# Optimization experiments

Hardware: AMD Instinct MI355X
Metric: run time of the kernel (lower is better)

The kernel has to match this reference:

```python
import jax, jax.numpy as jnp
import numpy as np

B, NQ, NC, C, NH, NP, DFF, HH, WW = 4, 300, 16, 256, 8, 4, 2048, 128, 128


def _ln(x, g, b):
    m = jnp.mean(x, -1, keepdims=True)
    v = jnp.mean((x - m) ** 2, -1, keepdims=True)
    return (x - m) / jnp.sqrt(v + 1e-5) * g + b


def _mha(x, wi, bi, wo, bo, n_heads):
    Bx, L, Cx = x.shape
    d = Cx // n_heads
    q, k, v = jnp.split(x @ wi.T + bi, 3, axis=-1)
    sh = lambda t: t.reshape(Bx, L, n_heads, d).transpose(0, 2, 1, 3)
    scale = float(1.0 / np.sqrt(d))
    a = jax.nn.softmax(jnp.einsum('bhqd,bhkd->bhqk', sh(q), sh(k)) * scale, axis=-1)
    o = jnp.einsum('bhqk,bhkd->bhqd', a, sh(v)).transpose(0, 2, 1, 3).reshape(Bx, L, Cx)
    return o @ wo.T + bo


def _grid_sample(im, grid):
    # im: [N, Ch, H, W]; grid: [N, L, P, 2] in [-1,1]; bilinear, zeros padding, align_corners=False
    N, Ch, H, W = im.shape
    gx = (grid[..., 0] + 1.0) * (W * 0.5) - 0.5
    gy = (grid[..., 1] + 1.0) * (H * 0.5) - 0.5
    x0 = jnp.floor(gx)
    y0 = jnp.floor(gy)
    wx1 = gx - x0
    wy1 = gy - y0
    imf = im.reshape(N, Ch, H * W)

    def gather(xi, yi):
        valid = ((xi >= 0) & (xi < W) & (yi >= 0) & (yi < H)).astype(im.dtype)
        idx = jnp.clip(yi, 0, H - 1).astype(jnp.int32) * W + jnp.clip(xi, 0, W - 1).astype(jnp.int32)
        vals = jnp.take_along_axis(imf, idx.reshape(N, 1, -1), axis=2).reshape(N, Ch, *xi.shape[1:])
        return vals * valid[:, None]

    return (gather(x0, y0) * ((1 - wx1) * (1 - wy1))[:, None]
            + gather(x0 + 1, y0) * (wx1 * (1 - wy1))[:, None]
            + gather(x0, y0 + 1) * ((1 - wx1) * wy1)[:, None]
            + gather(x0 + 1, y0 + 1) * (wx1 * wy1)[:, None])


def setup_inputs() -> dict:
    key = jax.random.key(0)
    ks = jax.random.split(key, 30)
    s = 0.02
    p = lambda k, shp: jax.random.normal(k, shp, jnp.float32) * s
    cxcy = jax.random.uniform(ks[0], (B, NQ * NC, 2), jnp.float32)
    wh = jax.random.uniform(ks[1], (B, NQ * NC, 2), jnp.float32) * 0.2 + 0.02
    return {
        'inst_query': jax.random.normal(ks[2], (B, NQ, C), jnp.float32),
        'sub_contour_query': jax.random.normal(ks[3], (B, NQ, NC, C), jnp.float32),
        'memory_feats': jax.random.normal(ks[4], (B, HH * WW, C), jnp.float32),
        'reference_boxes': jnp.concatenate([cxcy, wh], axis=-1),
        'inst_in_w': p(ks[5], (3 * C, C)), 'inst_in_b': p(ks[6], (3 * C,)),
        'inst_out_w': p(ks[7], (C, C)), 'inst_out_b': p(ks[8], (C,)),
        'sc_in_w': p(ks[9], (3 * C, C)), 'sc_in_b': p(ks[10], (3 * C,)),
        'sc_out_w': p(ks[11], (C, C)), 'sc_out_b': p(ks[12], (C,)),
        'off_w': p(ks[13], (NH * NP * 2, C)), 'off_b': p(ks[14], (NH * NP * 2,)),
        'aw_w': p(ks[15], (NH * NP, C)), 'aw_b': p(ks[16], (NH * NP,)),
        'outp_w': p(ks[17], (C, C)), 'outp_b': p(ks[18], (C,)),
        'lin1_w': p(ks[19], (DFF, C)), 'lin1_b': p(ks[20], (DFF,)),
        'lin2_w': p(ks[21], (C, DFF)), 'lin2_b': p(ks[22], (C,)),
        'n1_g': jnp.ones((C,), jnp.float32), 'n1_b': jnp.zeros((C,), jnp.float32),
        'n2_g': jnp.ones((C,), jnp.float32), 'n2_b': jnp.zeros((C,), jnp.float32),
        'n3_g': jnp.ones((C,), jnp.float32), 'n3_b': jnp.zeros((C,), jnp.float32),
        'H': HH, 'W': WW,
    }


def reference(inst_query, sub_contour_query, memory_feats, reference_boxes,
              inst_in_w, inst_in_b, inst_out_w, inst_out_b,
              sc_in_w, sc_in_b, sc_out_w, sc_out_b,
              off_w, off_b, aw_w, aw_b, outp_w, outp_b,
              lin1_w, lin1_b, lin2_w, lin2_b,
              n1_g, n1_b, n2_g, n2_b, n3_g, n3_b, H, W):
    Bx, Nq, Nc, Cx = sub_contour_query.shape
    Lq = Nq * Nc
    hd = Cx // NH
    # --- decoupled self-attention (eval mode: dropout = identity) ---
    inst_o = _mha(inst_query, inst_in_w, inst_in_b, inst_out_w, inst_out_b, NH)
    sc = sub_contour_query.transpose(0, 2, 1, 3).reshape(Bx * Nc, Nq, Cx)
    sc_o = _mha(sc, sc_in_w, sc_in_b, sc_out_w, sc_out_b, NH)
    sc_o = sc_o.reshape(Bx, Nc, Nq, Cx).transpose(0, 2, 1, 3)
    q_sa = sc_o + inst_o[:, :, None, :]
    tgt = (sub_contour_query + q_sa).reshape(Bx, Lq, Cx)
    tgt = _ln(tgt + q_sa.reshape(Bx, Lq, Cx), n1_g, n1_b)
    # --- deformable cross-attention ---
    offsets = (tgt @ off_w.T + off_b).reshape(Bx, Lq, NH, NP, 2)
    aw = jax.nn.softmax((tgt @ aw_w.T + aw_b).reshape(Bx, Lq, NH, NP), axis=-1)
    ref = reference_boxes[:, :, None, None, :]
    loc = ref[..., :2] + offsets * ref[..., 2:] * 0.5
    grid = (loc * 2.0 - 1.0).transpose(0, 2, 1, 3, 4).reshape(Bx * NH, Lq, NP, 2)
    mem = memory_feats.reshape(Bx, H, W, Cx).transpose(0, 3, 1, 2).reshape(Bx * NH, hd, H, W)
    samp = _grid_sample(mem, grid).reshape(Bx, NH, hd, Lq, NP).transpose(0, 3, 1, 4, 2)  # [B,Lq,nH,nP,hd]
    tgt2 = (samp * aw[..., None]).sum(3).reshape(Bx, Lq, Cx) @ outp_w.T + outp_b
    tgt = _ln(tgt + tgt2, n2_g, n2_b)
    # --- FFN ---
    tgt2 = jax.nn.relu(tgt @ lin1_w.T + lin1_b) @ lin2_w.T + lin2_b
    tgt = _ln(tgt + tgt2, n3_g, n3_b)
    return tgt.reshape(Bx, Nq, Nc, Cx)
```

## Files before the change

kernel.cpp:

```cpp
#include <hip/hip_runtime.h>
#include <hip/hip_bf16.h>
#include <math.h>


typedef unsigned short u16;
typedef unsigned int u32;
typedef __attribute__((ext_vector_type(4))) float f32x4;
typedef __attribute__((ext_vector_type(8))) short s16x8;

__device__ __forceinline__ float b2f(u16 u) {
    union { u32 u; float f; } v; v.u = ((u32)u) << 16; return v.f;
}
__device__ __forceinline__ u16 f2b(float f) {
    union { float f; u32 u; } v; v.f = f;
    u32 r = v.u + 0x7fffu + ((v.u >> 16) & 1u);
    return (u16)(r >> 16);
}
__device__ __forceinline__ u32 pkbf(float a, float b) {
    u32 r;
    asm("v_cvt_pk_bf16_f32 %0, %1, %2" : "=v"(r) : "v"(a), "v"(b));
    return r;
}

#define GLOAD_LDS16(g, l) \
    __builtin_amdgcn_global_load_lds((const __attribute__((address_space(1))) void*)(g), \
                                     (__attribute__((address_space(3))) void*)(l), 16, 0, 0)

struct CvtSeg { const float* src; u16* dst; int nv; };
struct Cvt8 { CvtSeg s[8]; };

__global__ __launch_bounds__(256) void cvt_multi(Cvt8 a, int totalv) {
    int v = blockIdx.x * 256 + threadIdx.x;
    if (v >= totalv) return;
    int si = 0;
    while (si < 7 && v >= a.s[si].nv) { v -= a.s[si].nv; ++si; }
    const float* src = a.s[si].src + (size_t)v * 8;
    u16* dst = a.s[si].dst + (size_t)v * 8;
    float4 x = *(const float4*)src;
    float4 y = *(const float4*)(src + 4);
    u16 u[8] = { f2b(x.x), f2b(x.y), f2b(x.z), f2b(x.w),
                 f2b(y.x), f2b(y.y), f2b(y.z), f2b(y.w) };
    *(uint4*)dst = *(const uint4*)u;
}

__global__ __launch_bounds__(256) void pack_offaw(
    const float* __restrict__ off_w, const float* __restrict__ off_b,
    const float* __restrict__ aw_w, const float* __restrict__ aw_b,
    u16* __restrict__ wout, float* __restrict__ bout)
{
    int r = blockIdx.x, c = threadIdx.x;
    float v = 0.f;
    if (r < 64) v = off_w[r * 256 + c];
    else if (r < 96) v = aw_w[(r - 64) * 256 + c];
    wout[r * 256 + c] = f2b(v);
    if (c == 0) bout[r] = (r < 64) ? off_b[r] : (r < 96 ? aw_b[r - 64] : 0.f);
}

template<int RELU, int OUTBF16, int TM>
__global__ __launch_bounds__(256) void gemm_mfma(
    const u16* __restrict__ A, const u16* __restrict__ W,
    const float* __restrict__ bias, void* __restrict__ Cout,
    int M, int N, int K)
{
    constexpr int MI = TM / 32;
    constexpr int CHA = TM * 64 / 2048;
    constexpr int CHB = 4;
    __shared__ u16 smem[(TM + 128) * 64];
    u16* Asm = smem;
    u16* Bsm = smem + TM * 64;
    const int tid = threadIdx.x;
    const int wave = tid >> 6, lane = tid & 63;
    const int gx = gridDim.x;
    const int nwg = gx * gridDim.y;
    const int lid = blockIdx.y * gx + blockIdx.x;
    const int q8 = nwg >> 3, r8 = nwg & 7;
    const int xcd = lid & 7, sub = lid >> 3;
    const int logical = (xcd < r8 ? xcd * (q8 + 1) : r8 * (q8 + 1) + (xcd - r8) * q8) + sub;
    const int bm = (logical / gx) * TM, bn = (logical % gx) * 128;
    const int wr = (wave >> 1) * (TM / 2), wc = (wave & 1) * 64;
    const int fr = lane & 15;
    const int g = lane >> 4;
    const int sw = fr & 7;
    f32x4 acc[MI][4] = {};

    for (int k0 = 0; k0 < K; k0 += 64) {
        __syncthreads();
#pragma unroll
        for (int c = 0; c < CHA; ++c) {
            int L = c * 256 + tid;
            int r = L >> 3, p = L & 7;
            int cc = p ^ (r & 7);
            int ra = bm + r; if (ra >= M) ra = M - 1;
            GLOAD_LDS16(A + (size_t)ra * K + k0 + cc * 8, Asm + (c * 256 + wave * 64) * 8);
        }
#pragma unroll
        for (int c = 0; c < CHB; ++c) {
            int L = c * 256 + tid;
            int r = L >> 3, p = L & 7;
            int cc = p ^ (r & 7);
            int rb = bn + r;
            GLOAD_LDS16(W + (size_t)rb * K + k0 + cc * 8, Bsm + (c * 256 + wave * 64) * 8);
        }
        __syncthreads();
#pragma unroll
        for (int kk = 0; kk < 2; ++kk) {
            const int pc = (kk * 4 + g) ^ sw;
            s16x8 af[MI], bf[4];
#pragma unroll
            for (int i = 0; i < MI; ++i)
                af[i] = *(const s16x8*)(Asm + (wr + i * 16 + fr) * 64 + pc * 8);
#pragma unroll
            for (int i = 0; i < 4; ++i)
                bf[i] = *(const s16x8*)(Bsm + (wc + i * 16 + fr) * 64 + pc * 8);
#pragma unroll
            for (int mi = 0; mi < MI; ++mi)
#pragma unroll
                for (int ni = 0; ni < 4; ++ni)
                    acc[mi][ni] = __builtin_amdgcn_mfma_f32_16x16x32_bf16(
                        af[mi], bf[ni], acc[mi][ni], 0, 0, 0);
        }
    }
    const int cc = lane & 15, cr4 = (lane >> 4) * 4;
    if (OUTBF16) {
#pragma unroll
        for (int p = 0; p < TM / 32; ++p) {
            const int base = p * 32;
            __syncthreads();
#pragma unroll
            for (int mi = 0; mi < MI; ++mi) {
                int rowoff = wr + mi * 16;
                if (rowoff < base || rowoff >= base + 32) continue;
#pragma unroll
                for (int ni = 0; ni < 4; ++ni) {
                    int col = wc + ni * 16 + cc;
                    float bv = bias[bn + col];
#pragma unroll
                    for (int j = 0; j < 4; ++j) {
                        float v = acc[mi][ni][j] + bv;
                        if (RELU) v = fmaxf(v, 0.f);
                        smem[(rowoff - base + cr4 + j) * 136 + col] = f2b(v);
                    }
                }
            }
            __syncthreads();
            for (int t = tid; t < 512; t += 256) {
                int row = t >> 4, ck = t & 15;
                int grow = bm + base + row;
                if (grow < M)
                    *(uint4*)((u16*)Cout + (size_t)grow * N + bn + ck * 8) =
                        *(const uint4*)&smem[row * 136 + ck * 8];
            }
        }
    } else {
#pragma unroll
        for (int mi = 0; mi < MI; ++mi) {
#pragma unroll
            for (int ni = 0; ni < 4; ++ni) {
                int col = bn + wc + ni * 16 + cc;
                float bv = bias[col];
#pragma unroll
                for (int j = 0; j < 4; ++j) {
                    int row = bm + wr + mi * 16 + cr4 + j;
                    if (row >= M) continue;
                    float v = acc[mi][ni][j] + bv;
                    if (RELU) v = fmaxf(v, 0.f);
                    ((float*)Cout)[(size_t)row * N + col] = v;
                }
            }
        }
    }
}

#define VIDX(d, k) ((((k) >> 3) ^ ((d) & 7)) * 8 + ((k) & 7))

__global__ __launch_bounds__(256) void attn_mfma(
    const u16* __restrict__ qkv, u16* __restrict__ O, int S)
{
    const int bh = blockIdx.x / S, seg = blockIdx.x % S;
    const int bi = bh >> 3, h = bh & 7;
    __shared__ u16 Ks[320][40];
    __shared__ u16 Vt[32][384];
    const int tid = threadIdx.x;

    for (int idx = tid; idx < 1200; idx += 256) {
        int k = idx >> 2, sub = idx & 3;
        const u16* kp = qkv + ((size_t)(bi * 300 + k)) * 768 + 256 + h * 32 + sub * 8;
        *(uint4*)&Ks[k][sub * 8] = *(const uint4*)kp;
    }
    for (int idx = tid; idx < 600; idx += 256) {
        int kp2 = idx >> 2, sub = idx & 3;
        int k0 = kp2 * 2;
        const u16* vp = qkv + ((size_t)(bi * 300 + k0)) * 768 + 512 + h * 32 + sub * 8;
        uint4 v0 = *(const uint4*)vp;
        uint4 v1 = *(const uint4*)(vp + 768);
        u16 a0[8], a1[8];
        *(uint4*)a0 = v0; *(uint4*)a1 = v1;
#pragma unroll
        for (int j = 0; j < 8; ++j) {
            int d = sub * 8 + j;
            *(u32*)&Vt[d][VIDX(d, k0)] = (u32)a0[j] | ((u32)a1[j] << 16);
        }
    }
    for (int idx = tid; idx < 320; idx += 256) {
        int d = idx & 31, k0 = 300 + (idx >> 5) * 2;
        *(u32*)&Vt[d][VIDX(d, k0)] = 0;
    }
    __syncthreads();

    const int lane = tid & 63, wave = tid >> 6;
    const int c = lane & 15, g = lane >> 4;
    const int fk = g * 8;
    const f32x4 zero = { 0.f, 0.f, 0.f, 0.f };
    const float SCL2 = 0.25505416f;
    const int sA = c + ((g & 1) << 5);
    const int sB = sA + 16;
    const bool hi = g >= 2;

    for (int qt = seg * 4 + wave; qt < 19; qt += 4 * S) {
        int qrow = qt * 16 + c; if (qrow > 299) qrow = 299;
        s16x8 afq = *(const s16x8*)(qkv + ((size_t)(bi * 300 + qrow)) * 768 + h * 32 + fk);
        f32x4 acc0 = zero, acc1 = zero;
        float m = -1e30f, l = 0.f;

        for (int kc = 0; kc < 10; ++kc) {
            const int kb = kc * 32;
            s16x8 ak0 = *(const s16x8*)&Ks[kb + c][fk];
            s16x8 ak1 = *(const s16x8*)&Ks[kb + 16 + c][fk];
            __builtin_amdgcn_s_setprio(1);
            f32x4 s0 = __builtin_amdgcn_mfma_f32_16x16x32_bf16(ak0, afq, zero, 0, 0, 0);
            f32x4 s1 = __builtin_amdgcn_mfma_f32_16x16x32_bf16(ak1, afq, zero, 0, 0, 0);
            __builtin_amdgcn_s_setprio(0);
            if (kb == 288) {
#pragma unroll
                for (int j = 0; j < 4; ++j) {
                    if (g == 3) s0[j] = -1e30f;
                    s1[j] = -1e30f;
                }
            }
            float cm = fmaxf(fmaxf(fmaxf(s0[0], s0[1]), fmaxf(s0[2], s0[3])),
                             fmaxf(fmaxf(s1[0], s1[1]), fmaxf(s1[2], s1[3])));
            cm = fmaxf(cm, __shfl_xor(cm, 16));
            cm = fmaxf(cm, __shfl_xor(cm, 32));
            float mn = fmaxf(m, cm);
            float corr = exp2f((m - mn) * SCL2);
            m = mn;
            float p0[4], p1[4];
#pragma unroll
            for (int j = 0; j < 4; ++j) {
                p0[j] = exp2f((s0[j] - m) * SCL2);
                p1[j] = exp2f((s1[j] - m) * SCL2);
            }
            float cs = (p0[0] + p0[1]) + (p0[2] + p0[3])
                     + (p1[0] + p1[1]) + (p1[2] + p1[3]);
            cs += __shfl_xor(cs, 16);
            cs += __shfl_xor(cs, 32);
            l = l * corr + cs;
            u32 w0 = pkbf(p0[0], p0[1]), w1 = pkbf(p0[2], p0[3]);
            u32 w2 = pkbf(p1[0], p1[1]), w3 = pkbf(p1[2], p1[3]);
            int x0 = __shfl((int)w0, sA), x1 = __shfl((int)w1, sA);
            int x2 = __shfl((int)w2, sA), x3 = __shfl((int)w3, sA);
            int y0 = __shfl((int)w0, sB), y1 = __shfl((int)w1, sB);
            int y2 = __shfl((int)w2, sB), y3 = __shfl((int)w3, sB);
            union { u32 w[4]; s16x8 v; } afp;
            afp.w[0] = hi ? (u32)x2 : (u32)x0;
            afp.w[1] = hi ? (u32)x3 : (u32)x1;
            afp.w[2] = hi ? (u32)y2 : (u32)y0;
            afp.w[3] = hi ? (u32)y3 : (u32)y1;
            float c0 = __shfl(corr, g * 4 + 0), c1 = __shfl(corr, g * 4 + 1);
            float c2 = __shfl(corr, g * 4 + 2), c3 = __shfl(corr, g * 4 + 3);
            acc0[0] *= c0; acc0[1] *= c1; acc0[2] *= c2; acc0[3] *= c3;
            acc1[0] *= c0; acc1[1] *= c1; acc1[2] *= c2; acc1[3] *= c3;
            s16x8 bv0 = *(const s16x8*)&Vt[c][VIDX(c, kb + fk)];
            s16x8 bv1 = *(const s16x8*)&Vt[16 + c][VIDX(16 + c, kb + fk)];
            __builtin_amdgcn_s_setprio(1);
            acc0 = __builtin_amdgcn_mfma_f32_16x16x32_bf16(afp.v, bv0, acc0, 0, 0, 0);
            acc1 = __builtin_amdgcn_mfma_f32_16x16x32_bf16(afp.v, bv1, acc1, 0, 0, 0);
            __builtin_amdgcn_s_setprio(0);
        }
        float l0 = __shfl(l, g * 4 + 0), l1 = __shfl(l, g * 4 + 1);
        float l2 = __shfl(l, g * 4 + 2), l3 = __shfl(l, g * 4 + 3);
        float lj[4] = { l0, l1, l2, l3 };
#pragma unroll
        for (int j = 0; j < 4; ++j) {
            int q = qt * 16 + g * 4 + j;
            if (q < 300) {
                float r = 1.f / lj[j];
                u16* op = O + ((size_t)(bi * 300 + q)) * 256 + h * 32;
                op[c]      = f2b(acc0[j] * r);
                op[16 + c] = f2b(acc1[j] * r);
            }
        }
    }
}

__global__ __launch_bounds__(256) void sc_transpose(
    const float* __restrict__ scq, u16* __restrict__ out)
{
    int row = blockIdx.x * 4 + (threadIdx.x >> 6);
    int c4 = (threadIdx.x & 63) * 4;
    int b = row / 4800;
    int rem = row % 4800;
    int nc = rem / 300, nq = rem % 300;
    float4 v = *(const float4*)(scq + ((size_t)((b * 300 + nq) * 16 + nc)) * 256 + c4);
    u16 u[4] = { f2b(v.x), f2b(v.y), f2b(v.z), f2b(v.w) };
    *(uint2*)(out + (size_t)row * 256 + c4) = *(const uint2*)u;
}

__global__ __launch_bounds__(256) void ln1_combine(
    const float* __restrict__ scq, const float* __restrict__ sco,
    const float* __restrict__ insto, const float* __restrict__ g,
    const float* __restrict__ bta, float* __restrict__ tgt,
    u16* __restrict__ tgtb)
{
    int row = blockIdx.x * 4 + (threadIdx.x >> 6);
    int c4 = (threadIdx.x & 63) * 4;
    int b = row / 4800;
    int rem = row % 4800;
    int nq = rem >> 4, nc = rem & 15;
    float4 a = *(const float4*)(scq + (size_t)row * 256 + c4);
    float4 s = *(const float4*)(sco + ((size_t)((b * 16 + nc) * 300 + nq)) * 256 + c4);
    float4 i = *(const float4*)(insto + ((size_t)(b * 300 + nq)) * 256 + c4);
    float4 v = { a.x + 2.f * (s.x + i.x), a.y + 2.f * (s.y + i.y),
                 a.z + 2.f * (s.z + i.z), a.w + 2.f * (s.w + i.w) };
    float sm = v.x + v.y + v.z + v.w;
    float s2 = v.x * v.x + v.y * v.y + v.z * v.z + v.w * v.w;
#pragma unroll
    for (int o = 32; o; o >>= 1) { sm += __shfl_xor(sm, o); s2 += __shfl_xor(s2, o); }
    float mean = sm * (1.f / 256.f);
    float rstd = 1.f / sqrtf(s2 * (1.f / 256.f) - mean * mean + 1e-5f);
    float4 gv = *(const float4*)(g + c4);
    float4 bv = *(const float4*)(bta + c4);
    float4 r = { (v.x - mean) * rstd * gv.x + bv.x, (v.y - mean) * rstd * gv.y + bv.y,
                 (v.z - mean) * rstd * gv.z + bv.z, (v.w - mean) * rstd * gv.w + bv.w };
    *(float4*)(tgt + (size_t)row * 256 + c4) = r;
    u16 u[4] = { f2b(r.x), f2b(r.y), f2b(r.z), f2b(r.w) };
    *(uint2*)(tgtb + (size_t)row * 256 + c4) = *(const uint2*)u;
}

__global__ __launch_bounds__(256) void ln_add(
    const float* __restrict__ x, const float* __restrict__ y,
    const float* __restrict__ g, const float* __restrict__ bta,
    float* __restrict__ dst, u16* __restrict__ bdst)
{
    int row = blockIdx.x * 4 + (threadIdx.x >> 6);
    int c4 = (threadIdx.x & 63) * 4;
    float4 a = *(const float4*)(x + (size_t)row * 256 + c4);
    float4 b = *(const float4*)(y + (size_t)row * 256 + c4);
    float4 v = { a.x + b.x, a.y + b.y, a.z + b.z, a.w + b.w };
    float sm = v.x + v.y + v.z + v.w;
    float s2 = v.x * v.x + v.y * v.y + v.z * v.z + v.w * v.w;
#pragma unroll
    for (int o = 32; o; o >>= 1) { sm += __shfl_xor(sm, o); s2 += __shfl_xor(s2, o); }
    float mean = sm * (1.f / 256.f);
    float rstd = 1.f / sqrtf(s2 * (1.f / 256.f) - mean * mean + 1e-5f);
    float4 gv = *(const float4*)(g + c4);
    float4 bv = *(const float4*)(bta + c4);
    float4 r = { (v.x - mean) * rstd * gv.x + bv.x, (v.y - mean) * rstd * gv.y + bv.y,
                 (v.z - mean) * rstd * gv.z + bv.z, (v.w - mean) * rstd * gv.w + bv.w };
    *(float4*)(dst + (size_t)row * 256 + c4) = r;
    if (bdst) {
        u16 u[4] = { f2b(r.x), f2b(r.y), f2b(r.z), f2b(r.w) };
        *(uint2*)(bdst + (size_t)row * 256 + c4) = *(const uint2*)u;
    }
}

__global__ __launch_bounds__(256) void deform_sample(
    const float* __restrict__ oaw, const float* __restrict__ refb,
    const float* __restrict__ mem, u16* __restrict__ samp)
{
    const int row = blockIdx.x;
    const int b = row / 4800;
    const int tid = threadIdx.x;
    const int h = tid >> 5;
    const float4 rb = *(const float4*)(refb + (size_t)row * 4);
    const float* base = oaw + (size_t)row * 128;
    float a0 = base[64 + h * 4 + 0], a1 = base[64 + h * 4 + 1];
    float a2 = base[64 + h * 4 + 2], a3 = base[64 + h * 4 + 3];
    float am = fmaxf(fmaxf(a0, a1), fmaxf(a2, a3));
    float e0 = __expf(a0 - am), e1 = __expf(a1 - am), e2 = __expf(a2 - am), e3 = __expf(a3 - am);
    float rs = 1.f / (e0 + e1 + e2 + e3);
    float wp[4] = { e0 * rs, e1 * rs, e2 * rs, e3 * rs };
    const float* op = base + h * 8;
    const float* mb = mem + (size_t)b * 16384 * 256 + tid;

    int offs[16];
    float wts[16];
#pragma unroll
    for (int p = 0; p < 4; ++p) {
        float gx = (rb.x + op[p * 2 + 0] * rb.z * 0.5f) * 128.f - 0.5f;
        float gy = (rb.y + op[p * 2 + 1] * rb.w * 0.5f) * 128.f - 0.5f;
        float x0f = floorf(gx), y0f = floorf(gy);
        int x0 = (int)x0f, y0 = (int)y0f;
        float wx1 = gx - x0f, wy1 = gy - y0f;
        float wx0 = 1.f - wx1, wy0 = 1.f - wy1;
        float vx0 = ((unsigned)x0 < 128u) ? 1.f : 0.f;
        float vx1 = ((unsigned)(x0 + 1) < 128u) ? 1.f : 0.f;
        float vy0 = ((unsigned)y0 < 128u) ? 1.f : 0.f;
        float vy1 = ((unsigned)(y0 + 1) < 128u) ? 1.f : 0.f;
        int xc0 = min(max(x0, 0), 127), xc1 = min(max(x0 + 1, 0), 127);
        int yc0 = min(max(y0, 0), 127), yc1 = min(max(y0 + 1, 0), 127);
        offs[p * 4 + 0] = (yc0 * 128 + xc0) << 8;
        offs[p * 4 + 1] = (yc0 * 128 + xc1) << 8;
        offs[p * 4 + 2] = (yc1 * 128 + xc0) << 8;
        offs[p * 4 + 3] = (yc1 * 128 + xc1) << 8;
        wts[p * 4 + 0] = wp[p] * wx0 * wy0 * vx0 * vy0;
        wts[p * 4 + 1] = wp[p] * wx1 * wy0 * vx1 * vy0;
        wts[p * 4 + 2] = wp[p] * wx0 * wy1 * vx0 * vy1;
        wts[p * 4 + 3] = wp[p] * wx1 * wy1 * vx1 * vy1;
    }
    float vals[16];
#pragma unroll
    for (int i = 0; i < 16; ++i) vals[i] = mb[offs[i]];
    float acc = 0.f;
#pragma unroll
    for (int i = 0; i < 16; ++i) acc = fmaf(vals[i], wts[i], acc);
    samp[(size_t)row * 256 + tid] = f2b(acc);
}

extern "C" void kernel_launch(void* const* d_in, const int* in_sizes, int n_in,
                              void* d_out, int out_size, void* d_ws, size_t ws_size,
                              hipStream_t stream) {
    const float* inst_query = (const float*)d_in[0];
    const float* sub_contour = (const float*)d_in[1];
    const float* memory_feats = (const float*)d_in[2];
    const float* ref_boxes = (const float*)d_in[3];
    const float* inst_in_w = (const float*)d_in[4];
    const float* inst_in_b = (const float*)d_in[5];
    const float* inst_out_w = (const float*)d_in[6];
    const float* inst_out_b = (const float*)d_in[7];
    const float* sc_in_w = (const float*)d_in[8];
    const float* sc_in_b = (const float*)d_in[9];
    const float* sc_out_w = (const float*)d_in[10];
    const float* sc_out_b = (const float*)d_in[11];
    const float* off_w = (const float*)d_in[12];
    const float* off_b = (const float*)d_in[13];
    const float* aw_w = (const float*)d_in[14];
    const float* aw_b = (const float*)d_in[15];
    const float* outp_w = (const float*)d_in[16];
    const float* outp_b = (const float*)d_in[17];
    const float* lin1_w = (const float*)d_in[18];
    const float* lin1_b = (const float*)d_in[19];
    const float* lin2_w = (const float*)d_in[20];
    const float* lin2_b = (const float*)d_in[21];
    const float* n1_g = (const float*)d_in[22];
    const float* n1_b = (const float*)d_in[23];
    const float* n2_g = (const float*)d_in[24];
    const float* n2_b = (const float*)d_in[25];
    const float* n3_g = (const float*)d_in[26];
    const float* n3_b = (const float*)d_in[27];

    u16* wsb = (u16*)d_ws;
    u16* qkv_b   = wsb;
    u16* xbuf_b  = qkv_b + 14745600;
    u16* obuf_b  = xbuf_b + 4915200;
    u16* tgt_b   = obuf_b + 4915200;
    u16* w_inst_in  = tgt_b + 4915200;
    u16* w_inst_out = w_inst_in + 196608;
    u16* w_sc_in    = w_inst_out + 65536;
    u16* w_sc_out   = w_sc_in + 196608;
    u16* w_outp     = w_sc_out + 65536;
    u16* w_lin1     = w_outp + 65536;
    u16* w_lin2     = w_lin1 + 524288;
    u16* w_offaw    = w_lin2 + 524288;
    u16* ffn1_b = qkv_b;
    u16* instq_b = tgt_b;
    float* fp    = (float*)(w_offaw + 32768);
    float* insto = fp;
    float* tgt   = insto + 307200;
    float* t2    = tgt + 4915200;
    float* oawb  = t2 + 4915200;
    float* b_offaw = oawb + 2457600;
    size_t base_bytes = (size_t)((char*)(b_offaw + 128) - (char*)d_ws);
    size_t ffn_off = (base_bytes + 255) & ~(size_t)255;
    u16* ffn1_full = (u16*)((char*)d_ws + ffn_off);
    bool full_ffn = ws_size >= ffn_off + (size_t)2 * 19200 * 2048;

    dim3 blk(256);

    Cvt8 ca;
    ca.s[0] = { inst_in_w,  w_inst_in,  196608 / 8 };
    ca.s[1] = { inst_out_w, w_inst_out, 65536 / 8 };
    ca.s[2] = { sc_in_w,    w_sc_in,    196608 / 8 };
    ca.s[3] = { sc_out_w,   w_sc_out,   65536 / 8 };
    ca.s[4] = { outp_w,     w_outp,     65536 / 8 };
    ca.s[5] = { lin1_w,     w_lin1,     524288 / 8 };
    ca.s[6] = { lin2_w,     w_lin2,     524288 / 8 };
    ca.s[7] = { inst_query, instq_b,    307200 / 8 };
    int totalv = (196608 * 2 + 65536 * 3 + 524288 * 2 + 307200) / 8;
    cvt_multi<<<(totalv + 255) / 256, blk, 0, stream>>>(ca, totalv);
    pack_offaw<<<128, blk, 0, stream>>>(off_w, off_b, aw_w, aw_b, w_offaw, b_offaw);

    gemm_mfma<0,1,128><<<dim3(6, 10), blk, 0, stream>>>(instq_b, w_inst_in, inst_in_b, qkv_b, 1200, 768, 256);
    attn_mfma<<<128, blk, 0, stream>>>(qkv_b, obuf_b, 4);
    gemm_mfma<0,0,64><<<dim3(2, 19), blk, 0, stream>>>(obuf_b, w_inst_out, inst_out_b, insto, 1200, 256, 256);
    sc_transpose<<<4800, blk, 0, stream>>>(sub_contour, xbuf_b);
    gemm_mfma<0,1,128><<<dim3(6, 150), blk, 0, stream>>>(xbuf_b, w_sc_in, sc_in_b, qkv_b, 19200, 768, 256);
    attn_mfma<<<1024, blk, 0, stream>>>(qkv_b, obuf_b, 2);
    gemm_mfma<0,0,64><<<dim3(2, 300), blk, 0, stream>>>(obuf_b, w_sc_out, sc_out_b, t2, 19200, 256, 256);
    ln1_combine<<<4800, blk, 0, stream>>>(sub_contour, t2, insto, n1_g, n1_b, tgt, tgt_b);
    gemm_mfma<0,0,64><<<dim3(1, 300), blk, 0, stream>>>(tgt_b, w_offaw, b_offaw, oawb, 19200, 128, 256);
    deform_sample<<<19200, blk, 0, stream>>>(oawb, ref_boxes, memory_feats, obuf_b);
    gemm_mfma<0,0,64><<<dim3(2, 300), blk, 0, stream>>>(obuf_b, w_outp, outp_b, t2, 19200, 256, 256);
    ln_add<<<4800, blk, 0, stream>>>(tgt, t2, n2_g, n2_b, tgt, tgt_b);
    if (full_ffn) {
        gemm_mfma<1,1,128><<<dim3(16, 150), blk, 0, stream>>>(tgt_b, w_lin1, lin1_b, ffn1_full, 19200, 2048, 256);
        gemm_mfma<0,0,64><<<dim3(2, 300), blk, 0, stream>>>(ffn1_full, w_lin2, lin2_b, t2, 19200, 256, 2048);
    } else {
        for (int c = 0; c < 2; ++c) {
            gemm_mfma<1,1,128><<<dim3(16, 75), blk, 0, stream>>>(tgt_b + (size_t)c * 9600 * 256, w_lin1, lin1_b, ffn1_b, 9600, 2048, 256);
            gemm_mfma<0,0,64><<<dim3(2, 150), blk, 0, stream>>>(ffn1_b, w_lin2, lin2_b, t2 + (size_t)c * 9600 * 256, 9600, 256, 2048);
        }
    }
    ln_add<<<4800, blk, 0, stream>>>(tgt, t2, n3_g, n3_b, (float*)d_out, nullptr);
}
```

Measured before the change: 319.6 us.

## Replace online softmax with two-pass full-row softmax in self-attention kernel

The attention kernel now computes all ten QK score tiles up front and keeps them in registers. It takes a single row max, then does exp and PV accumulation without per-chunk max correction, rescaling or cross-lane shuffles. The V-transpose LDS buffer shrinks to 320 columns and gets a new XOR swizzle that also depends on the upper bits of d, meant to cut bank conflicts. Holding 80 score floats per lane raises register pressure, which could hurt occupancy.

```diff
diff --git a/kernel.cpp b/kernel.cpp
--- a/kernel.cpp
+++ b/kernel.cpp
@@ -171,7 +171,8 @@
     }
 }
 
-#define VIDX(d, k) ((((k) >> 3) ^ ((d) & 7)) * 8 + ((k) & 7))
+#define T4(s) ((((s) << 1) ^ (s)) & 7)
+#define VIDX(d, k) (((((k) >> 3) ^ ((d) & 7) ^ T4((d) >> 3)) << 3) + ((k) & 7))
 
 __global__ __launch_bounds__(256) void attn_mfma(
     const u16* __restrict__ qkv, u16* __restrict__ O, int S)
@@ -179,7 +180,7 @@
     const int bh = blockIdx.x / S, seg = blockIdx.x % S;
     const int bi = bh >> 3, h = bh & 7;
     __shared__ u16 Ks[320][40];
-    __shared__ u16 Vt[32][384];
+    __shared__ u16 Vt[32][320];
     const int tid = threadIdx.x;
 
     for (int idx = tid; idx < 1200; idx += 256) {
@@ -219,42 +220,44 @@
     for (int qt = seg * 4 + wave; qt < 19; qt += 4 * S) {
         int qrow = qt * 16 + c; if (qrow > 299) qrow = 299;
         s16x8 afq = *(const s16x8*)(qkv + ((size_t)(bi * 300 + qrow)) * 768 + h * 32 + fk);
+        f32x4 s0[10], s1[10];
+        __builtin_amdgcn_s_setprio(1);
+#pragma unroll
+        for (int kc = 0; kc < 10; ++kc) {
+            s16x8 ak0 = *(const s16x8*)&Ks[kc * 32 + c][fk];
+            s16x8 ak1 = *(const s16x8*)&Ks[kc * 32 + 16 + c][fk];
+            s0[kc] = __builtin_amdgcn_mfma_f32_16x16x32_bf16(ak0, afq, zero, 0, 0, 0);
+            s1[kc] = __builtin_amdgcn_mfma_f32_16x16x32_bf16(ak1, afq, zero, 0, 0, 0);
+        }
+        __builtin_amdgcn_s_setprio(0);
+#pragma unroll
+        for (int j = 0; j < 4; ++j) {
+            if (g == 3) s0[9][j] = -1e30f;
+            s1[9][j] = -1e30f;
+        }
+        f32x4 mv = s0[0];
+#pragma unroll
+        for (int kc = 0; kc < 10; ++kc)
+#pragma unroll
+            for (int j = 0; j < 4; ++j) {
+                if (kc) mv[j] = fmaxf(mv[j], s0[kc][j]);
+                mv[j] = fmaxf(mv[j], s1[kc][j]);
+            }
+        float m = fmaxf(fmaxf(mv[0], mv[1]), fmaxf(mv[2], mv[3]));
+        m = fmaxf(m, __shfl_xor(m, 16));
+        m = fmaxf(m, __shfl_xor(m, 32));
         f32x4 acc0 = zero, acc1 = zero;
-        float m = -1e30f, l = 0.f;
-
+        float l = 0.f;
+#pragma unroll
         for (int kc = 0; kc < 10; ++kc) {
             const int kb = kc * 32;
-            s16x8 ak0 = *(const s16x8*)&Ks[kb + c][fk];
-            s16x8 ak1 = *(const s16x8*)&Ks[kb + 16 + c][fk];
-            __builtin_amdgcn_s_setprio(1);
-            f32x4 s0 = __builtin_amdgcn_mfma_f32_16x16x32_bf16(ak0, afq, zero, 0, 0, 0);
-            f32x4 s1 = __builtin_amdgcn_mfma_f32_16x16x32_bf16(ak1, afq, zero, 0, 0, 0);
-            __builtin_amdgcn_s_setprio(0);
-            if (kb == 288) {
-#pragma unroll
-                for (int j = 0; j < 4; ++j) {
-                    if (g == 3) s0[j] = -1e30f;
-                    s1[j] = -1e30f;
-                }
+            float p0[4], p1[4];
+#pragma unroll
+            for (int j = 0; j < 4; ++j) {
+                p0[j] = exp2f((s0[kc][j] - m) * SCL2);
+                p1[j] = exp2f((s1[kc][j] - m) * SCL2);
             }
-            float cm = fmaxf(fmaxf(fmaxf(s0[0], s0[1]), fmaxf(s0[2], s0[3])),
-                             fmaxf(fmaxf(s1[0], s1[1]), fmaxf(s1[2], s1[3])));
-            cm = fmaxf(cm, __shfl_xor(cm, 16));
-            cm = fmaxf(cm, __shfl_xor(cm, 32));
-            float mn = fmaxf(m, cm);
-            float corr = exp2f((m - mn) * SCL2);
-            m = mn;
-            float p0[4], p1[4];
-#pragma unroll
-            for (int j = 0; j < 4; ++j) {
-                p0[j] = exp2f((s0[j] - m) * SCL2);
-                p1[j] = exp2f((s1[j] - m) * SCL2);
-            }
-            float cs = (p0[0] + p0[1]) + (p0[2] + p0[3])
-                     + (p1[0] + p1[1]) + (p1[2] + p1[3]);
-            cs += __shfl_xor(cs, 16);
-            cs += __shfl_xor(cs, 32);
-            l = l * corr + cs;
+            l += (p0[0] + p0[1]) + (p0[2] + p0[3]) + (p1[0] + p1[1]) + (p1[2] + p1[3]);
             u32 w0 = pkbf(p0[0], p0[1]), w1 = pkbf(p0[2], p0[3]);
             u32 w2 = pkbf(p1[0], p1[1]), w3 = pkbf(p1[2], p1[3]);
             int x0 = __shfl((int)w0, sA), x1 = __shfl((int)w1, sA);
@@ -266,10 +269,6 @@
             afp.w[1] = hi ? (u32)x3 : (u32)x1;
             afp.w[2] = hi ? (u32)y2 : (u32)y0;
             afp.w[3] = hi ? (u32)y3 : (u32)y1;
-            float c0 = __shfl(corr, g * 4 + 0), c1 = __shfl(corr, g * 4 + 1);
-            float c2 = __shfl(corr, g * 4 + 2), c3 = __shfl(corr, g * 4 + 3);
-            acc0[0] *= c0; acc0[1] *= c1; acc0[2] *= c2; acc0[3] *= c3;
-            acc1[0] *= c0; acc1[1] *= c1; acc1[2] *= c2; acc1[3] *= c3;
             s16x8 bv0 = *(const s16x8*)&Vt[c][VIDX(c, kb + fk)];
             s16x8 bv1 = *(const s16x8*)&Vt[16 + c][VIDX(16 + c, kb + fk)];
             __builtin_amdgcn_s_setprio(1);
@@ -277,6 +276,8 @@
             acc1 = __builtin_amdgcn_mfma_f32_16x16x32_bf16(afp.v, bv1, acc1, 0, 0, 0);
             __builtin_amdgcn_s_setprio(0);
         }
+        l += __shfl_xor(l, 16);
+        l += __shfl_xor(l, 32);
         float l0 = __shfl(l, g * 4 + 0), l1 = __shfl(l, g * 4 + 1);
         float l2 = __shfl(l, g * 4 + 2), l3 = __shfl(l, g * 4 + 3);
         float lj[4] = { l0, l1, l2, l3 };
```

After: 321.7 us. No clear change (+0.6%).
